# Kernel tuning notes

Measured on AMD Instinct MI355X. Metric: run time of the kernel, lower is better.

The kernel has to match this reference:

```python
import jax, jax.numpy as jnp
import numpy as np

B, T, D, K = 16, 1024, 256, 1024
DECAY = 0.99
EPS = 1e-5


def setup_inputs() -> dict:
    key = jax.random.key(0)
    k1, k2 = jax.random.split(key)
    x = jax.random.normal(k1, (B, T, D), dtype=jnp.float32)
    # nn.Embedding weight initialized uniform(-1/num_emb, 1/num_emb)
    embed_w = jax.random.uniform(k2, (K, D), dtype=jnp.float32,
                                 minval=-1.0 / K, maxval=1.0 / K)
    ema_cluster_size = jnp.zeros((K,), dtype=jnp.float32)
    ema_w = embed_w  # self._ema_w = embed.weight.clone()
    return {"x": x, "embed_w": embed_w,
            "ema_cluster_size": ema_cluster_size, "ema_w": ema_w}


def reference(x, embed_w, ema_cluster_size, ema_w):
    input_shape = x.shape
    flat = x.reshape(-1, input_shape[-1])          # [N, D]
    N = flat.shape[0]

    dist = (jnp.sum(flat * flat, axis=1, keepdims=True)
            + jnp.sum(embed_w * embed_w, axis=1)[None, :]
            - 2.0 * jnp.matmul(flat, embed_w.T))
    idx = jnp.argmin(dist, axis=-1)                # [N] int32

    # one_hot @ W  ==  gather rows of codebook
    quant_flat = embed_w[idx]                      # [N, D]
    # straight-through estimator (custom backward passes grad to input only)
    quant_flat = flat + jax.lax.stop_gradient(quant_flat - flat)
    quantized = quant_flat.reshape(input_shape)

    # ---- training-mode EMA updates (enc_idx.sum(0) == counts; enc_idx.T @ flat == segment_sum) ----
    counts = jax.ops.segment_sum(jnp.ones((N,), dtype=flat.dtype), idx,
                                 num_segments=K)
    cs = ema_cluster_size * DECAY + (1.0 - DECAY) * counts
    n = jnp.sum(cs)
    cs = (cs + EPS) / (n + K * EPS) * n
    dw = jax.ops.segment_sum(flat, idx, num_segments=K)   # [K, D]
    ema_w_new = ema_w * DECAY + (1.0 - DECAY) * dw
    embed_new = ema_w_new / cs[:, None]

    # commitment loss (quantized detached)
    e_latent_loss = jnp.mean((x - jax.lax.stop_gradient(quantized)) ** 2)
    loss = 0.25 * e_latent_loss

    return quantized, loss, embed_new, cs, ema_w_new
```

## Files before the change

### kernel.cpp

```cpp
#include <hip/hip_runtime.h>
#include <cstdint>
#include <cstddef>

namespace {
constexpr int NROW = 16384;
constexpr int KC   = 1024;
constexpr int DIM  = 256;
constexpr int MT   = 128;
constexpr int KSPLIT = 8;
constexpr int KPB  = KC / KSPLIT;
constexpr int FCAP = 8192;
constexpr int RPB  = 4;
}

typedef __attribute__((ext_vector_type(8))) short bf16x8;
typedef __attribute__((ext_vector_type(4))) float f32x4;
typedef unsigned long long u64;
typedef uint32_t u32;

__device__ __forceinline__ unsigned fkey(float s) {
  unsigned u = __float_as_uint(s);
  return ((int)u >= 0) ? (u ^ 0x80000000u) : ~u;
}
__device__ __forceinline__ float unfkey(unsigned u) {
  return __uint_as_float((u & 0x80000000u) ? (u ^ 0x80000000u) : ~u);
}

__device__ __forceinline__ void split2(float a, u32& h, u32& l) {
  const u32 u  = __float_as_uint(a);
  const u32 rh = (u + 0x7fffu + ((u >> 16) & 1u)) >> 16;
  const float ah = __uint_as_float(rh << 16);
  const float al = a - ah;
  const u32 v  = __float_as_uint(al);
  const u32 rl = (v + 0x7fffu + ((v >> 16) & 1u)) >> 16;
  h = rh & 0xffffu; l = rl & 0xffffu;
}

__device__ __forceinline__ float np_sumsq_256(const float* __restrict__ p) {
  float half[2];
  #pragma unroll
  for (int h = 0; h < 2; h++) {
    const float* q = p + h * 128;
    float r[8];
    #pragma unroll
    for (int j = 0; j < 8; j++) r[j] = __fmul_rn(q[j], q[j]);
    #pragma unroll 1
    for (int i = 8; i < 128; i += 8)
      #pragma unroll
      for (int j = 0; j < 8; j++)
        r[j] = __fadd_rn(r[j], __fmul_rn(q[i + j], q[i + j]));
    half[h] = __fadd_rn(__fadd_rn(__fadd_rn(r[0], r[1]), __fadd_rn(r[2], r[3])),
                        __fadd_rn(__fadd_rn(r[4], r[5]), __fadd_rn(r[6], r[7])));
  }
  return __fadd_rn(half[0], half[1]);
}

__global__ __launch_bounds__(256)
void pack_wnorm_kernel(const float4* __restrict__ x4, const float4* __restrict__ w4,
                       const float* __restrict__ w,
                       uint4* __restrict__ xh4, uint4* __restrict__ xl4,
                       uint4* __restrict__ wh4, uint4* __restrict__ wl4,
                       float* __restrict__ wnorm) {
  if (blockIdx.x >= 2176) {
    const int k = (blockIdx.x - 2176) * 256 + threadIdx.x;
    wnorm[k] = np_sumsq_256(&w[k * DIM]);
    return;
  }
  const int g = blockIdx.x * 256 + threadIdx.x;
  const float4* src; uint4* dh; uint4* dl; int gg;
  if (g < 524288) { gg = g;          src = x4; dh = xh4; dl = xl4; }
  else            { gg = g - 524288; src = w4; dh = wh4; dl = wl4; }
  const float4 a = src[gg * 2], b = src[gg * 2 + 1];
  u32 h[8], l[8];
  split2(a.x, h[0], l[0]); split2(a.y, h[1], l[1]);
  split2(a.z, h[2], l[2]); split2(a.w, h[3], l[3]);
  split2(b.x, h[4], l[4]); split2(b.y, h[5], l[5]);
  split2(b.z, h[6], l[6]); split2(b.w, h[7], l[7]);
  uint4 H, L;
  H.x = h[0] | (h[1] << 16); H.y = h[2] | (h[3] << 16);
  H.z = h[4] | (h[5] << 16); H.w = h[6] | (h[7] << 16);
  L.x = l[0] | (l[1] << 16); L.y = l[2] | (l[3] << 16);
  L.z = l[4] | (l[5] << 16); L.w = l[6] | (l[7] << 16);
  dh[gg] = H; dl[gg] = L;
}

__global__ __launch_bounds__(256, 3)
void dist_mfma_kernel(const ushort* __restrict__ xh, const ushort* __restrict__ xl,
                      const ushort* __restrict__ wh, const ushort* __restrict__ wl,
                      const float* __restrict__ wnorm,
                      u64* __restrict__ pairs) {
  __shared__ __align__(16) u32 lds[8192];

  const int tid  = threadIdx.x;
  const int lane = tid & 63;
  const int wv   = tid >> 6;
  const int quad = lane >> 4;
  const int idx16 = lane & 15;
  const int bid  = blockIdx.x;
  const int rowBase = (((bid >> 6) << 3) | (bid & 7)) * MT;
  const int sp      = (bid >> 3) & 7;
  const int kbase   = sp * KPB;

  const int subrow = lane >> 2, grp = lane & 3;
  const ushort* gptr[8];
  u32 ldst[8];
  #pragma unroll
  for (int j = 0; j < 8; j++) {
    const int c = wv * 8 + j;
    const ushort* plane; int r0; u32 dstB;
    if (c < 8)       { plane = xh + rowBase * DIM; r0 = c * 16;        dstB = c * 1024; }
    else if (c < 16) { plane = xl + rowBase * DIM; r0 = (c - 8) * 16;  dstB = 8192 + (c - 8) * 1024; }
    else if (c < 24) { plane = wh + kbase * DIM;   r0 = (c - 16) * 16; dstB = 16384 + (c - 16) * 1024; }
    else             { plane = wl + kbase * DIM;   r0 = (c - 24) * 16; dstB = 24576 + (c - 24) * 1024; }
    gptr[j] = plane + (r0 + subrow) * DIM + grp * 8;
    ldst[j] = dstB >> 2;
  }

  f32x4 acc[2][8];
  #pragma unroll
  for (int rt = 0; rt < 2; rt++)
    #pragma unroll
    for (int ct = 0; ct < 8; ct++) acc[rt][ct] = (f32x4){0.f, 0.f, 0.f, 0.f};

  #pragma unroll 1
  for (int kc = 0; kc < DIM / 32; kc++) {
    __syncthreads();
    #pragma unroll
    for (int j = 0; j < 8; j++) {
      __builtin_amdgcn_global_load_lds(
          (const __attribute__((address_space(1))) u32*)(gptr[j]),
          (__attribute__((address_space(3))) u32*)&lds[ldst[j]], 16, 0, 0);
      gptr[j] += 32;
    }
    __syncthreads();

    bf16x8 Ah[2], Al[2];
    #pragma unroll
    for (int rt = 0; rt < 2; rt++) {
      const int ar = wv * 32 + rt * 16 + idx16;
      Ah[rt] = *(const bf16x8*)((const char*)lds + ar * 64 + quad * 16);
      Al[rt] = *(const bf16x8*)((const char*)lds + 8192 + ar * 64 + quad * 16);
    }
    #pragma unroll
    for (int ct = 0; ct < 8; ct++) {
      const int br = ct * 16 + idx16;
      const bf16x8 Bh = *(const bf16x8*)((const char*)lds + 16384 + br * 64 + quad * 16);
      const bf16x8 Bl = *(const bf16x8*)((const char*)lds + 24576 + br * 64 + quad * 16);
      #pragma unroll
      for (int rt = 0; rt < 2; rt++) {
        acc[rt][ct] = __builtin_amdgcn_mfma_f32_16x16x32_bf16(Al[rt], Bh, acc[rt][ct], 0, 0, 0);
        acc[rt][ct] = __builtin_amdgcn_mfma_f32_16x16x32_bf16(Ah[rt], Bl, acc[rt][ct], 0, 0, 0);
        acc[rt][ct] = __builtin_amdgcn_mfma_f32_16x16x32_bf16(Ah[rt], Bh, acc[rt][ct], 0, 0, 0);
      }
    }
  }

  u64 b0[2][4], b1[2][4];
  #pragma unroll
  for (int rt = 0; rt < 2; rt++)
    #pragma unroll
    for (int reg = 0; reg < 4; reg++) { b0[rt][reg] = ~0ULL; b1[rt][reg] = ~0ULL; }

  #pragma unroll
  for (int ct = 0; ct < 8; ct++) {
    const int col = kbase + ct * 16 + idx16;
    const float wn = wnorm[col];
    #pragma unroll
    for (int rt = 0; rt < 2; rt++) {
      #pragma unroll
      for (int reg = 0; reg < 4; reg++) {
        const float s = fmaf(-2.0f, acc[rt][ct][reg], wn);
        const u64 p = ((u64)fkey(s) << 32) | (unsigned)col;
        if (p < b1[rt][reg]) {
          if (p < b0[rt][reg]) { b1[rt][reg] = b0[rt][reg]; b0[rt][reg] = p; }
          else                 { b1[rt][reg] = p; }
        }
      }
    }
  }

  #pragma unroll
  for (int m = 1; m <= 8; m <<= 1) {
    #pragma unroll
    for (int rt = 0; rt < 2; rt++) {
      #pragma unroll
      for (int reg = 0; reg < 4; reg++) {
        const u64 o0 = __shfl_xor(b0[rt][reg], m);
        const u64 o1 = __shfl_xor(b1[rt][reg], m);
        if (o0 < b0[rt][reg]) {
          b1[rt][reg] = (b0[rt][reg] < o1) ? b0[rt][reg] : o1;
          b0[rt][reg] = o0;
        } else {
          b1[rt][reg] = (b1[rt][reg] < o0) ? b1[rt][reg] : o0;
        }
      }
    }
  }

  if (idx16 == 0) {
    #pragma unroll
    for (int rt = 0; rt < 2; rt++) {
      #pragma unroll
      for (int reg = 0; reg < 4; reg++) {
        const int row = rowBase + wv * 32 + rt * 16 + quad * 4 + reg;
        pairs[row * 16 + sp * 2 + 0] = b0[rt][reg];
        pairs[row * 16 + sp * 2 + 1] = b1[rt][reg];
      }
    }
  }
}

__global__ __launch_bounds__(256)
void merge_kernel(const u64* __restrict__ pairs,
                  int* __restrict__ idx, float* __restrict__ counts,
                  int* __restrict__ flags, int* __restrict__ counter) {
  const int row = blockIdx.x * 256 + threadIdx.x;
  const u64* p = &pairs[row * 16];
  u64 B0 = p[0], B1 = p[1];
  #pragma unroll
  for (int s = 1; s < KSPLIT; s++) {
    const u64 c0 = p[s * 2], c1 = p[s * 2 + 1];
    if (c0 < B0) { B1 = (B0 < c1) ? B0 : c1; B0 = c0; }
    else         { B1 = (B1 < c0) ? B1 : c0; }
  }
  const int k = (int)(B0 & 0xffffffffULL);
  idx[row] = k;
  atomicAdd(&counts[k], 1.0f);
  const float s0 = unfkey((unsigned)(B0 >> 32));
  const float s1 = unfkey((unsigned)(B1 >> 32));
  if (s1 - s0 < 2e-4f) {
    const int pos = atomicAdd(counter, 1);
    if (pos < FCAP) flags[pos] = row;
  }
}

__global__ __launch_bounds__(256)
void recheck_np_kernel(const float* __restrict__ x, const float* __restrict__ w,
                       const float* __restrict__ wnorm,
                       const int* __restrict__ flags, const int* __restrict__ counter,
                       int* __restrict__ idx, float* __restrict__ counts) {
  __shared__ float xs[RPB][DIM];
  __shared__ float x2sh[RPB];
  __shared__ u64 red[RPB][256];

  const int cnt  = min(*counter, FCAP);
  const int base = blockIdx.x * RPB;
  if (base >= cnt) return;
  const int nr = min(RPB, cnt - base);

  #pragma unroll
  for (int r = 0; r < RPB; r++)
    xs[r][threadIdx.x] = (r < nr) ? x[flags[base + r] * DIM + threadIdx.x] : 0.0f;
  __syncthreads();
  if (threadIdx.x < RPB) x2sh[threadIdx.x] = np_sumsq_256(xs[threadIdx.x]);
  __syncthreads();
  double x2d[RPB];
  #pragma unroll
  for (int r = 0; r < RPB; r++) x2d[r] = (double)x2sh[r];

  u64 best[RPB];
  #pragma unroll
  for (int r = 0; r < RPB; r++) best[r] = ~0ULL;

  #pragma unroll 1
  for (int g = 0; g < 4; g++) {
    const int k = threadIdx.x * 4 + g;
    const float* wr = &w[k * DIM];
    const double w2 = (double)wnorm[k];
    double dot[RPB];
    #pragma unroll
    for (int r = 0; r < RPB; r++) dot[r] = 0.0;
    #pragma unroll 1
    for (int d = 0; d < DIM; d += 4) {
      const float4 wv = *(const float4*)&wr[d];
      #pragma unroll
      for (int r = 0; r < RPB; r++) {
        dot[r] = fma((double)xs[r][d],     (double)wv.x, dot[r]);
        dot[r] = fma((double)xs[r][d + 1], (double)wv.y, dot[r]);
        dot[r] = fma((double)xs[r][d + 2], (double)wv.z, dot[r]);
        dot[r] = fma((double)xs[r][d + 3], (double)wv.w, dot[r]);
      }
    }
    #pragma unroll
    for (int r = 0; r < RPB; r++) {
      const float mmf = (float)dot[r];
      const float S1  = (float)(x2d[r] + w2);
      const float D   = (float)((double)S1 - 2.0 * (double)mmf);
      const u64 key = ((u64)fkey(D) << 32) | (unsigned)k;
      if (key < best[r]) best[r] = key;
    }
  }

  #pragma unroll
  for (int r = 0; r < RPB; r++) red[r][threadIdx.x] = best[r];
  __syncthreads();
  #pragma unroll
  for (int off = 128; off > 0; off >>= 1) {
    if ((int)threadIdx.x < off) {
      #pragma unroll
      for (int r = 0; r < RPB; r++) {
        const u64 o = red[r][threadIdx.x + off];
        if (o < red[r][threadIdx.x]) red[r][threadIdx.x] = o;
      }
    }
    __syncthreads();
  }
  if ((int)threadIdx.x < nr) {
    const int row  = flags[base + threadIdx.x];
    const int newk = (int)(red[threadIdx.x][0] & 0xffffffffULL);
    const int oldk = idx[row];
    if (newk != oldk) {
      idx[row] = newk;
      atomicAdd(&counts[newk],  1.0f);
      atomicAdd(&counts[oldk], -1.0f);
    }
  }
}

__global__ __launch_bounds__(1024)
void prefix_cs_kernel(const float* __restrict__ ema_cs, const float* __restrict__ counts,
                      int* __restrict__ starts, int* __restrict__ cursor,
                      float* __restrict__ out_cs, float* __restrict__ cs_ws) {
  __shared__ int sc[1024];
  __shared__ float lds[17];
  const int t = threadIdx.x;
  const int ci = (int)counts[t];
  sc[t] = ci;
  const float c = ema_cs[t] * 0.99f + 0.01f * counts[t];
  float v = c;
  #pragma unroll
  for (int off = 32; off > 0; off >>= 1) v += __shfl_down(v, off);
  if ((t & 63) == 0) lds[t >> 6] = v;
  __syncthreads();
  if (t == 0) {
    float n = 0.0f;
    for (int i = 0; i < 16; i++) n += lds[i];
    lds[16] = n;
  }
  __syncthreads();
  const float n = lds[16];
  const float csv = (c + 1e-5f) / (n + 1024.0f * 1e-5f) * n;
  out_cs[t] = csv;
  cs_ws[t]  = csv;
  #pragma unroll
  for (int off = 1; off < 1024; off <<= 1) {
    const int add = (t >= off) ? sc[t - off] : 0;
    __syncthreads();
    sc[t] += add;
    __syncthreads();
  }
  const int excl = sc[t] - ci;
  starts[t] = excl;
  cursor[t] = excl;
}

__global__ __launch_bounds__(256)
void scatter_kernel(const int* __restrict__ idx, int* __restrict__ cursor,
                    int* __restrict__ bucket) {
  const int row = blockIdx.x * 256 + threadIdx.x;
  const int k = idx[row];
  const int pos = atomicAdd(&cursor[k], 1);
  bucket[pos] = row;
}

__global__ __launch_bounds__(256)
void dw_bucket_kernel(const float4* __restrict__ x4, const int* __restrict__ bucket,
                      const int* __restrict__ starts, const float* __restrict__ counts,
                      float4* __restrict__ dw4) {
  __shared__ float4 red[4][64];
  const int k   = blockIdx.x;
  const int d4  = threadIdx.x & 63;
  const int rg  = threadIdx.x >> 6;
  const int s   = starts[k];
  const int e   = s + (int)counts[k];
  float4 acc = {0.f, 0.f, 0.f, 0.f};
  for (int i = s + rg; i < e; i += 4) {
    const float4 v = x4[bucket[i] * 64 + d4];
    acc.x += v.x; acc.y += v.y; acc.z += v.z; acc.w += v.w;
  }
  red[rg][d4] = acc;
  __syncthreads();
  if (rg == 0) {
    const float4 a1 = red[1][d4], a2 = red[2][d4], a3 = red[3][d4];
    acc.x += a1.x + a2.x + a3.x;
    acc.y += a1.y + a2.y + a3.y;
    acc.z += a1.z + a2.z + a3.z;
    acc.w += a1.w + a2.w + a3.w;
    dw4[k * 64 + d4] = acc;
  }
}

__global__ __launch_bounds__(256)
void quant_loss_kernel(const float4* __restrict__ x4,
                       const float4* __restrict__ w4,
                       const int* __restrict__ idx,
                       float4* __restrict__ outq,
                       float* __restrict__ partials) {
  __shared__ float lds[4];
  const int g  = blockIdx.x * 256 + threadIdx.x;
  const int n  = g >> 6;
  const int d4 = g & 63;
  const float4 xv = x4[g];
  const int   k  = idx[n];
  const float4 qv = w4[k * 64 + d4];
  float4 r;
  r.x = xv.x + (qv.x - xv.x);
  r.y = xv.y + (qv.y - xv.y);
  r.z = xv.z + (qv.z - xv.z);
  r.w = xv.w + (qv.w - xv.w);
  outq[g] = r;

  const float dx = xv.x - r.x, dy = xv.y - r.y, dz = xv.z - r.z, dwv = xv.w - r.w;
  float s = dx * dx + dy * dy + dz * dz + dwv * dwv;
  #pragma unroll
  for (int off = 32; off > 0; off >>= 1) s += __shfl_down(s, off);
  if ((threadIdx.x & 63) == 0) lds[threadIdx.x >> 6] = s;
  __syncthreads();
  if (threadIdx.x == 0) partials[blockIdx.x] = lds[0] + lds[1] + lds[2] + lds[3];
}

__global__ __launch_bounds__(256)
void emb_loss_kernel(const float* __restrict__ ema_w, const float* __restrict__ dw,
                     const float* __restrict__ cs, const float* __restrict__ partials,
                     float* __restrict__ out_ema_w, float* __restrict__ out_embed,
                     float* __restrict__ out_loss) {
  if (blockIdx.x == 1024) {
    __shared__ float lds[4];
    float s = 0.0f;
    for (int i = threadIdx.x; i < 4096; i += 256) s += partials[i];
    #pragma unroll
    for (int off = 32; off > 0; off >>= 1) s += __shfl_down(s, off);
    if ((threadIdx.x & 63) == 0) lds[threadIdx.x >> 6] = s;
    __syncthreads();
    if (threadIdx.x == 0) {
      const float total = lds[0] + lds[1] + lds[2] + lds[3];
      out_loss[0] = 0.25f * (total / 4194304.0f);
    }
    return;
  }
  const int g = blockIdx.x * 256 + threadIdx.x;
  const int k = g >> 8;
  const float e = ema_w[g] * 0.99f + 0.01f * dw[g];
  out_ema_w[g] = e;
  out_embed[g] = e / cs[k];
}

extern "C" void kernel_launch(void* const* d_in, const int* in_sizes, int n_in,
                              void* d_out, int out_size, void* d_ws, size_t ws_size,
                              hipStream_t stream) {
  const float* x       = (const float*)d_in[0];
  const float* embed_w = (const float*)d_in[1];
  const float* ema_cs  = (const float*)d_in[2];
  const float* ema_w   = (const float*)d_in[3];

  float* out        = (float*)d_out;
  float* out_q      = out;
  float* out_loss   = out + 4194304;
  float* out_embed  = out + 4194305;
  float* out_cs     = out + 4456449;
  float* out_ema_w  = out + 4457473;

  char* ws = (char*)d_ws;
  u64*   pairs    = (u64*)  (ws + 0);
  int*   bucket   = (int*)  (ws + 0);
  float* dw       = (float*)(ws + 1048576);
  int*   idx      = (int*)  (ws + 2097152);
  float* counts   = (float*)(ws + 2162688);
  int*   counter  = (int*)  (ws + 2166784);
  int*   flags    = (int*)  (ws + 2166912);
  float* wnorm    = (float*)(ws + 2199680);
  float* cs_ws    = (float*)(ws + 2203776);
  float* partials = (float*)(ws + 2207872);
  int*   starts   = (int*)  (ws + 2224256);
  int*   cursor   = (int*)  (ws + 2228352);
  ushort* wh      = (ushort*)(ws + 2232448);
  ushort* wl      = (ushort*)(ws + 2756736);

  ushort* xh = (ushort*)out_q;
  ushort* xl = (ushort*)out_q + 4194304;

  hipMemsetAsync(counts, 0, 4100, stream);

  pack_wnorm_kernel<<<2180, 256, 0, stream>>>(
      (const float4*)x, (const float4*)embed_w, embed_w,
      (uint4*)xh, (uint4*)xl, (uint4*)wh, (uint4*)wl, wnorm);
  dist_mfma_kernel<<<(NROW / MT) * KSPLIT, 256, 0, stream>>>(xh, xl, wh, wl, wnorm, pairs);
  merge_kernel<<<NROW / 256, 256, 0, stream>>>(pairs, idx, counts, flags, counter);
  recheck_np_kernel<<<FCAP / RPB, 256, 0, stream>>>(x, embed_w, wnorm, flags, counter,
                                                    idx, counts);
  prefix_cs_kernel<<<1, 1024, 0, stream>>>(ema_cs, counts, starts, cursor, out_cs, cs_ws);
  scatter_kernel<<<NROW / 256, 256, 0, stream>>>(idx, cursor, bucket);
  dw_bucket_kernel<<<KC, 256, 0, stream>>>((const float4*)x, bucket, starts, counts,
                                           (float4*)dw);
  quant_loss_kernel<<<NROW * 64 / 256, 256, 0, stream>>>(
      (const float4*)x, (const float4*)embed_w, idx, (float4*)out_q, partials);
  emb_loss_kernel<<<KC * DIM / 256 + 1, 256, 0, stream>>>(
      ema_w, dw, cs_ws, partials, out_ema_w, out_embed, out_loss);
}
```

Measured before the change: 206.2 us.

## Recheck near-tie rows with one codeword per thread and wave-shuffle argmin

```diff
diff --git a/kernel.cpp b/kernel.cpp
--- a/kernel.cpp
+++ b/kernel.cpp
@@ -234,85 +234,110 @@
   }
 }
 
-__global__ __launch_bounds__(256)
+__global__ __launch_bounds__(1024)
 void recheck_np_kernel(const float* __restrict__ x, const float* __restrict__ w,
                        const float* __restrict__ wnorm,
                        const int* __restrict__ flags, const int* __restrict__ counter,
                        int* __restrict__ idx, float* __restrict__ counts) {
-  __shared__ float xs[RPB][DIM];
-  __shared__ float x2sh[RPB];
-  __shared__ u64 red[RPB][256];
+  __shared__ float  xs[RPB][DIM];
+  __shared__ double xd[RPB][DIM];
+  __shared__ float  x2sh[RPB];
+  __shared__ u64    red[RPB][16];
 
   const int cnt  = min(*counter, FCAP);
   const int base = blockIdx.x * RPB;
   if (base >= cnt) return;
   const int nr = min(RPB, cnt - base);
 
-  #pragma unroll
-  for (int r = 0; r < RPB; r++)
-    xs[r][threadIdx.x] = (r < nr) ? x[flags[base + r] * DIM + threadIdx.x] : 0.0f;
+  {
+    const int r = threadIdx.x >> 8, d = threadIdx.x & 255;
+    const float v = (r < nr) ? x[flags[base + r] * DIM + d] : 0.0f;
+    xs[r][d] = v;
+    xd[r][d] = (double)v;
+  }
   __syncthreads();
   if (threadIdx.x < RPB) x2sh[threadIdx.x] = np_sumsq_256(xs[threadIdx.x]);
   __syncthreads();
+
   double x2d[RPB];
   #pragma unroll
   for (int r = 0; r < RPB; r++) x2d[r] = (double)x2sh[r];
 
-  u64 best[RPB];
-  #pragma unroll
-  for (int r = 0; r < RPB; r++) best[r] = ~0ULL;
+  const int k = threadIdx.x;
+  const float* __restrict__ wr = &w[k * DIM];
+  const double w2 = (double)wnorm[k];
+
+  double dot[RPB];
+  #pragma unroll
+  for (int r = 0; r < RPB; r++) dot[r] = 0.0;
+
+  float4 wv[4];
+  #pragma unroll
+  for (int q = 0; q < 4; q++) wv[q] = *(const float4*)&wr[q * 4];
 
   #pragma unroll 1
-  for (int g = 0; g < 4; g++) {
-    const int k = threadIdx.x * 4 + g;
-    const float* wr = &w[k * DIM];
-    const double w2 = (double)wnorm[k];
-    double dot[RPB];
-    #pragma unroll
-    for (int r = 0; r < RPB; r++) dot[r] = 0.0;
-    #pragma unroll 1
-    for (int d = 0; d < DIM; d += 4) {
-      const float4 wv = *(const float4*)&wr[d];
+  for (int d = 0; d < DIM; d += 16) {
+    float4 cur[4];
+    #pragma unroll
+    for (int q = 0; q < 4; q++) cur[q] = wv[q];
+    if (d + 16 < DIM) {
+      #pragma unroll
+      for (int q = 0; q < 4; q++) wv[q] = *(const float4*)&wr[d + 16 + q * 4];
+    }
+    #pragma unroll
+    for (int q = 0; q < 4; q++) {
+      const double wa = (double)cur[q].x, wb = (double)cur[q].y,
+                   wc = (double)cur[q].z, wd_ = (double)cur[q].w;
       #pragma unroll
       for (int r = 0; r < RPB; r++) {
-        dot[r] = fma((double)xs[r][d],     (double)wv.x, dot[r]);
-        dot[r] = fma((double)xs[r][d + 1], (double)wv.y, dot[r]);
-        dot[r] = fma((double)xs[r][d + 2], (double)wv.z, dot[r]);
-        dot[r] = fma((double)xs[r][d + 3], (double)wv.w, dot[r]);
+        dot[r] = fma(xd[r][d + q * 4 + 0], wa,  dot[r]);
+        dot[r] = fma(xd[r][d + q * 4 + 1], wb,  dot[r]);
+        dot[r] = fma(xd[r][d + q * 4 + 2], wc,  dot[r]);
+        dot[r] = fma(xd[r][d + q * 4 + 3], wd_, dot[r]);
       }
     }
+  }
+
+  u64 key[RPB];
+  #pragma unroll
+  for (int r = 0; r < RPB; r++) {
+    const float mmf = (float)dot[r];
+    const float S1  = (float)(x2d[r] + w2);
+    const float D   = (float)((double)S1 - 2.0 * (double)mmf);
+    key[r] = ((u64)fkey(D) << 32) | (unsigned)k;
+  }
+
+  #pragma unroll
+  for (int m = 1; m < 64; m <<= 1) {
     #pragma unroll
     for (int r = 0; r < RPB; r++) {
-      const float mmf = (float)dot[r];
-      const float S1  = (float)(x2d[r] + w2);
-      const float D   = (float)((double)S1 - 2.0 * (double)mmf);
-      const u64 key = ((u64)fkey(D) << 32) | (unsigned)k;
-      if (key < best[r]) best[r] = key;
-    }
-  }
-
-  #pragma unroll
-  for (int r = 0; r < RPB; r++) red[r][threadIdx.x] = best[r];
-  __syncthreads();
-  #pragma unroll
-  for (int off = 128; off > 0; off >>= 1) {
-    if ((int)threadIdx.x < off) {
-      #pragma unroll
-      for (int r = 0; r < RPB; r++) {
-        const u64 o = red[r][threadIdx.x + off];
-        if (o < red[r][threadIdx.x]) red[r][threadIdx.x] = o;
+      const u64 o = __shfl_xor(key[r], m);
+      if (o < key[r]) key[r] = o;
+    }
+  }
+  if ((threadIdx.x & 63) == 0) {
+    const int wid = threadIdx.x >> 6;
+    #pragma unroll
+    for (int r = 0; r < RPB; r++) red[r][wid] = key[r];
+  }
+  __syncthreads();
+  if (threadIdx.x < 64) {
+    const int r = threadIdx.x >> 4, l = threadIdx.x & 15;
+    u64 kk = red[r][l];
+    #pragma unroll
+    for (int m = 1; m < 16; m <<= 1) {
+      const u64 o = __shfl_xor(kk, m);
+      if (o < kk) kk = o;
+    }
+    if (l == 0 && r < nr) {
+      const int row  = flags[base + r];
+      const int newk = (int)(kk & 0xffffffffULL);
+      const int oldk = idx[row];
+      if (newk != oldk) {
+        idx[row] = newk;
+        atomicAdd(&counts[newk],  1.0f);
+        atomicAdd(&counts[oldk], -1.0f);
       }
-    }
-    __syncthreads();
-  }
-  if ((int)threadIdx.x < nr) {
-    const int row  = flags[base + threadIdx.x];
-    const int newk = (int)(red[threadIdx.x][0] & 0xffffffffULL);
-    const int oldk = idx[row];
-    if (newk != oldk) {
-      idx[row] = newk;
-      atomicAdd(&counts[newk],  1.0f);
-      atomicAdd(&counts[oldk], -1.0f);
     }
   }
 }
@@ -486,8 +511,8 @@
       (uint4*)xh, (uint4*)xl, (uint4*)wh, (uint4*)wl, wnorm);
   dist_mfma_kernel<<<(NROW / MT) * KSPLIT, 256, 0, stream>>>(xh, xl, wh, wl, wnorm, pairs);
   merge_kernel<<<NROW / 256, 256, 0, stream>>>(pairs, idx, counts, flags, counter);
-  recheck_np_kernel<<<FCAP / RPB, 256, 0, stream>>>(x, embed_w, wnorm, flags, counter,
-                                                    idx, counts);
+  recheck_np_kernel<<<FCAP / RPB, 1024, 0, stream>>>(x, embed_w, wnorm, flags, counter,
+                                                     idx, counts);
   prefix_cs_kernel<<<1, 1024, 0, stream>>>(ema_cs, counts, starts, cursor, out_cs, cs_ws);
   scatter_kernel<<<NROW / 256, 256, 0, stream>>>(idx, cursor, bucket);
   dw_bucket_kernel<<<KC, 256, 0, stream>>>((const float4*)x, bucket, starts, counts,
```

Result: faster. 194.3 us (-5.8%).
